# Kernel optimization log

Measured on AMD Instinct MI355X. Metric: run time of the kernel, lower is better.

Reference implementation:

```python
import jax, jax.numpy as jnp
import numpy as np

TAU = 0.5  # matches init_kwargs tau
EPS = 1e-8  # torch CosineSimilarity eps


def setup_inputs() -> dict:
    key = jax.random.key(0)
    k1, k2 = jax.random.split(key)
    B, D = 4096, 256
    return {
        "z_orig": jax.random.normal(k1, (B, D), dtype=jnp.float32),
        "z_augment": jax.random.normal(k2, (B, D), dtype=jnp.float32),
    }


def reference(z_orig, z_augment):
    B = z_orig.shape[0]
    N = 2 * B
    # collect_z = cat([z_augment, z_orig])  -> [2B, D]
    z = jnp.concatenate([z_augment, z_orig], axis=0)
    # cosine similarity matrix via L2 normalize + matmul
    zn = z / jnp.maximum(jnp.linalg.norm(z, axis=-1, keepdims=True), EPS)
    S = zn @ zn.T  # [2B, 2B]
    # positives: diag offsets +B and -B
    pos = jnp.concatenate([jnp.diagonal(S, B), jnp.diagonal(S, -B)])[:, None]  # [2B, 1]
    # negatives: everything except main diag and the +/-B diagonals.
    # Static indices (shape-dependent only), computed in numpy at trace time.
    mask = ~((np.eye(N, k=B) + np.eye(N, k=-B) + np.eye(N)).astype(bool))
    flat_idx = jnp.asarray(np.nonzero(mask.reshape(-1))[0])  # [2B*(2B-2)]
    neg = S.reshape(-1)[flat_idx].reshape(N, N - 2)  # row-major order matches torch boolean mask
    logits = jnp.concatenate([pos, neg], axis=1) / TAU  # [2B, 2B-1]
    # CrossEntropy with label 0 for every row, reduction='sum', then / 2B
    loss = -jax.nn.log_softmax(logits, axis=-1)[:, 0]
    return jnp.sum(loss) / N
```

## Files before the change

### kernel.cpp

```cpp
#include <hip/hip_runtime.h>
#include <hip/hip_bf16.h>

typedef __attribute__((ext_vector_type(4))) float f32x4;
typedef __attribute__((ext_vector_type(4))) int   i32x4;
typedef __attribute__((ext_vector_type(8))) int   i32x8;

#define N_ROWS 8192
#define B_HALF 4096
#define NUT   2080
#define EXP2C4 0.01127105500694503f
#define SCL1   0x7F7F7F7Fu

#define WS_ZN       0
#define WS_ROWACC   2097152
#define WS_POS      2129920
#define WS_DIAG     2162688
#define WS_ACC      2195456
#define WS_CNT      2195460

__device__ __forceinline__ float fexp2(float x) {
#if __has_builtin(__builtin_amdgcn_exp2f)
    return __builtin_amdgcn_exp2f(x);
#else
    return exp2f(x);
#endif
}

__device__ __forceinline__ unsigned int q4(float x) {
    float a = fabsf(x);
    unsigned int s = (__float_as_uint(x) >> 31) << 3;
    unsigned int c = a < 0.25f ? 0u : a < 0.75f ? 1u : a < 1.25f ? 2u
                   : a < 1.75f ? 3u : a < 2.5f  ? 4u : a < 3.5f  ? 5u
                   : a < 5.0f  ? 6u : 7u;
    return c | s;
}

__device__ __forceinline__ i32x8 widen(i32x4 v) {
    return (i32x8){v.x, v.y, v.z, v.w, 0, 0, 0, 0};
}

__device__ __forceinline__ float dpp_rowsum16(float x) {
    x += __int_as_float(__builtin_amdgcn_update_dpp(
             0, __float_as_int(x), 0x111, 0xF, 0xF, true));
    x += __int_as_float(__builtin_amdgcn_update_dpp(
             0, __float_as_int(x), 0x112, 0xF, 0xF, true));
    x += __int_as_float(__builtin_amdgcn_update_dpp(
             0, __float_as_int(x), 0x114, 0xF, 0xF, true));
    x += __int_as_float(__builtin_amdgcn_update_dpp(
             0, __float_as_int(x), 0x118, 0xF, 0xF, true));
    return x;
}

__global__ __launch_bounds__(256) void normalize_k(
    const float* __restrict__ z_orig, const float* __restrict__ z_aug,
    unsigned char* __restrict__ zn, float* __restrict__ rowAcc,
    float* __restrict__ accum, unsigned int* __restrict__ cnt)
{
    if (blockIdx.x == 0 && threadIdx.x == 0) { *accum = 0.0f; *cnt = 0u; }
    const int row  = blockIdx.x * 4 + (threadIdx.x >> 6);
    const int lane = threadIdx.x & 63;
    if (lane == 0) rowAcc[row] = 0.0f;
    const float* src = (row < B_HALF) ? (z_aug  + (size_t)row * 256)
                                      : (z_orig + (size_t)(row - B_HALF) * 256);
    float4 v = ((const float4*)src)[lane];
    float ss = v.x*v.x + v.y*v.y + v.z*v.z + v.w*v.w;
    #pragma unroll
    for (int m = 1; m < 64; m <<= 1) ss += __shfl_xor(ss, m);
    float inv = 16.0f / fmaxf(sqrtf(ss), 1e-8f);
    unsigned int pk = q4(v.x * inv) | (q4(v.y * inv) << 4)
                    | (q4(v.z * inv) << 8) | (q4(v.w * inv) << 12);
    const int addr = ((row >> 4) << 11) | ((lane >> 5) << 10) | ((row & 15) << 6)
                   | (((lane >> 3) & 3) << 4) | ((lane & 7) << 1);
    *(unsigned short*)(zn + addr) = (unsigned short)pk;
}

__global__ __launch_bounds__(256, 3) void tile_k(
    const unsigned char* __restrict__ zn,
    float* __restrict__ rowAcc,
    float* __restrict__ posv,
    float* __restrict__ diagE)
{
    const int bid = blockIdx.x;
    int rb = (int)((129.0f - sqrtf(16641.0f - 8.0f * (float)bid)) * 0.5f);
    rb = rb < 0 ? 0 : (rb > 63 ? 63 : rb);
    while ((rb + 1) * (129 - (rb + 1)) / 2 <= bid) ++rb;
    while (rb * (129 - rb) / 2 > bid) --rb;
    const int cb = rb + (bid - rb * (129 - rb) / 2);

    const int t      = threadIdx.x;
    const int lane   = t & 63;
    const int w      = t >> 6;
    const int wy     = w >> 1;
    const int wx     = w & 1;
    const int lane15 = lane & 15;
    const int quad   = lane >> 4;
    const int rowBase = rb * 128;
    const int colBase = cb * 128;

    const int laneOff = lane15 * 64 + quad * 16;
    const unsigned char* gA = zn + (size_t)(rb * 8 + wy * 4) * 2048 + laneOff;
    const unsigned char* gB = zn + (size_t)(cb * 8 + wx * 4) * 2048 + laneOff;

    f32x4 acc[4][4];
    #pragma unroll
    for (int i = 0; i < 4; ++i)
        #pragma unroll
        for (int j = 0; j < 4; ++j)
            acc[i][j] = (f32x4){0.f, 0.f, 0.f, 0.f};

    #pragma unroll
    for (int ks = 0; ks < 2; ++ks) {
        i32x4 a[4], b[4];
        #pragma unroll
        for (int mi = 0; mi < 4; ++mi)
            a[mi] = *(const i32x4*)(gA + mi * 2048 + ks * 1024);
        #pragma unroll
        for (int ni = 0; ni < 4; ++ni)
            b[ni] = *(const i32x4*)(gB + ni * 2048 + ks * 1024);
        #pragma unroll
        for (int mi = 0; mi < 4; ++mi)
            #pragma unroll
            for (int ni = 0; ni < 4; ++ni)
                acc[mi][ni] = __builtin_amdgcn_mfma_scale_f32_16x16x128_f8f6f4(
                    widen(a[mi]), widen(b[ni]), acc[mi][ni],
                    4, 4,
                    0, SCL1, 0, SCL1);
    }

    const bool diagLane = (wy == wx) && ((lane15 >> 2) == quad);
    const int  rsel = lane15 & 3;
    if (cb == rb && diagLane) {
        #pragma unroll
        for (int mi = 0; mi < 4; ++mi) {
            int grow = rowBase + wy * 64 + mi * 16 + lane15;
            diagE[grow] = fexp2(acc[mi][mi][rsel] * EXP2C4);
        }
    }
    if (cb == rb + 32 && diagLane) {
        #pragma unroll
        for (int mi = 0; mi < 4; ++mi) {
            int grow = rowBase + wy * 64 + mi * 16 + lane15;
            float v = acc[mi][mi][rsel];
            posv[grow] = v;
            posv[grow + B_HALF] = v;
        }
    }

    #pragma unroll
    for (int mi = 0; mi < 4; ++mi)
        #pragma unroll
        for (int ni = 0; ni < 4; ++ni)
            #pragma unroll
            for (int r = 0; r < 4; ++r)
                acc[mi][ni][r] = fexp2(acc[mi][ni][r] * EXP2C4);

    #pragma unroll
    for (int mi = 0; mi < 4; ++mi)
        #pragma unroll
        for (int r = 0; r < 4; ++r) {
            float s = acc[mi][0][r] + acc[mi][1][r] + acc[mi][2][r] + acc[mi][3][r];
            s = dpp_rowsum16(s);
            if (lane15 == 15)
                atomicAdd(&rowAcc[rowBase + wy * 64 + mi * 16 + quad * 4 + r], s);
        }

    if (cb != rb) {
        #pragma unroll
        for (int ni = 0; ni < 4; ++ni) {
            float s = 0.0f;
            #pragma unroll
            for (int mi = 0; mi < 4; ++mi)
                s += acc[mi][ni][0] + acc[mi][ni][1] + acc[mi][ni][2] + acc[mi][ni][3];
            s += __shfl_xor(s, 16);
            s += __shfl_xor(s, 32);
            if (quad == 0)
                atomicAdd(&rowAcc[colBase + wx * 64 + ni * 16 + lane15], s);
        }
    }
}

__global__ __launch_bounds__(256) void loss_k(
    const float* __restrict__ rowAcc, const float* __restrict__ posv,
    const float* __restrict__ diagE, float* __restrict__ accum,
    unsigned int* __restrict__ cnt, float* __restrict__ out)
{
    const int i = blockIdx.x * 256 + threadIdx.x;
    float s = rowAcc[i] - diagE[i];
    float loss = __logf(s) - posv[i] * 0.0078125f;

    #pragma unroll
    for (int m = 1; m < 64; m <<= 1) loss += __shfl_xor(loss, m);
    __shared__ float red[4];
    if ((threadIdx.x & 63) == 0) red[threadIdx.x >> 6] = loss;
    __syncthreads();
    if (threadIdx.x == 0) {
        float bs = red[0] + red[1] + red[2] + red[3];
        atomicAdd(accum, bs);
        __threadfence();
        unsigned int old = atomicAdd(cnt, 1u);
        if (old == 31u) {
            __threadfence();
            float total = atomicAdd(accum, 0.0f);
            out[0] = total * (1.0f / (float)N_ROWS);
        }
    }
}

extern "C" void kernel_launch(void* const* d_in, const int* in_sizes, int n_in,
                              void* d_out, int out_size, void* d_ws, size_t ws_size,
                              hipStream_t stream) {
    const float* z_orig = (const float*)d_in[0];
    const float* z_aug  = (const float*)d_in[1];
    char* ws = (char*)d_ws;
    unsigned char* zn   = (unsigned char*)(ws + WS_ZN);
    float* rowAcc       = (float*)(ws + WS_ROWACC);
    float* posv         = (float*)(ws + WS_POS);
    float* diagE        = (float*)(ws + WS_DIAG);
    float* accum        = (float*)(ws + WS_ACC);
    unsigned int* cnt   = (unsigned int*)(ws + WS_CNT);

    normalize_k<<<N_ROWS / 4, 256, 0, stream>>>(z_orig, z_aug, zn, rowAcc, accum, cnt);
    tile_k<<<NUT, 256, 0, stream>>>(zn, rowAcc, posv, diagE);
    loss_k<<<N_ROWS / 256, 256, 0, stream>>>(rowAcc, posv, diagE, accum, cnt,
                                             (float*)d_out);
}
```

Before: 92.94 us.

## Process two column tiles per block, reusing A fragments and prefetching next B

```diff
diff --git a/kernel.cpp b/kernel.cpp
--- a/kernel.cpp
+++ b/kernel.cpp
@@ -7,7 +7,6 @@
 
 #define N_ROWS 8192
 #define B_HALF 4096
-#define NUT   2080
 #define EXP2C4 0.01127105500694503f
 #define SCL1   0x7F7F7F7Fu
 
@@ -74,18 +73,75 @@
     *(unsigned short*)(zn + addr) = (unsigned short)pk;
 }
 
-__global__ __launch_bounds__(256, 3) void tile_k(
+__device__ __forceinline__ void do_epilogue(
+    f32x4 (&acc)[4][4], const int cb, const int rb, const int rowBase,
+    const int wy, const int wx, const int lane15, const int quad,
+    const bool diagLane, const int rsel,
+    float* __restrict__ rowAcc, float* __restrict__ posv,
+    float* __restrict__ diagE)
+{
+    const int colBase = cb * 128;
+    if (cb == rb && diagLane) {
+        #pragma unroll
+        for (int mi = 0; mi < 4; ++mi) {
+            int grow = rowBase + wy * 64 + mi * 16 + lane15;
+            diagE[grow] = fexp2(acc[mi][mi][rsel] * EXP2C4);
+        }
+    }
+    if (cb == rb + 32 && diagLane) {
+        #pragma unroll
+        for (int mi = 0; mi < 4; ++mi) {
+            int grow = rowBase + wy * 64 + mi * 16 + lane15;
+            float v = acc[mi][mi][rsel];
+            posv[grow] = v;
+            posv[grow + B_HALF] = v;
+        }
+    }
+
+    #pragma unroll
+    for (int mi = 0; mi < 4; ++mi)
+        #pragma unroll
+        for (int ni = 0; ni < 4; ++ni)
+            #pragma unroll
+            for (int r = 0; r < 4; ++r)
+                acc[mi][ni][r] = fexp2(acc[mi][ni][r] * EXP2C4);
+
+    #pragma unroll
+    for (int mi = 0; mi < 4; ++mi)
+        #pragma unroll
+        for (int r = 0; r < 4; ++r) {
+            float s = acc[mi][0][r] + acc[mi][1][r] + acc[mi][2][r] + acc[mi][3][r];
+            s = dpp_rowsum16(s);
+            if (lane15 == 15)
+                atomicAdd(&rowAcc[rowBase + wy * 64 + mi * 16 + quad * 4 + r], s);
+        }
+
+    if (cb != rb) {
+        #pragma unroll
+        for (int ni = 0; ni < 4; ++ni) {
+            float s = 0.0f;
+            #pragma unroll
+            for (int mi = 0; mi < 4; ++mi)
+                s += acc[mi][ni][0] + acc[mi][ni][1] + acc[mi][ni][2] + acc[mi][ni][3];
+            s += __shfl_xor(s, 16);
+            s += __shfl_xor(s, 32);
+            if (quad == 0)
+                atomicAdd(&rowAcc[colBase + wx * 64 + ni * 16 + lane15], s);
+        }
+    }
+}
+
+__global__ __launch_bounds__(256, 2) void tile_k(
     const unsigned char* __restrict__ zn,
     float* __restrict__ rowAcc,
     float* __restrict__ posv,
     float* __restrict__ diagE)
 {
-    const int bid = blockIdx.x;
-    int rb = (int)((129.0f - sqrtf(16641.0f - 8.0f * (float)bid)) * 0.5f);
-    rb = rb < 0 ? 0 : (rb > 63 ? 63 : rb);
-    while ((rb + 1) * (129 - (rb + 1)) / 2 <= bid) ++rb;
-    while (rb * (129 - rb) / 2 > bid) --rb;
-    const int cb = rb + (bid - rb * (129 - rb) / 2);
+    const int rb  = blockIdx.y;
+    const int cb0 = rb + 2 * (int)blockIdx.x;
+    if (cb0 > 63) return;
+    const int cb1 = cb0 + 1;
+    const bool have1 = (cb1 <= 63);
 
     const int t      = threadIdx.x;
     const int lane   = t & 63;
@@ -95,11 +151,22 @@
     const int lane15 = lane & 15;
     const int quad   = lane >> 4;
     const int rowBase = rb * 128;
-    const int colBase = cb * 128;
+    const bool diagLane = (wy == wx) && ((lane15 >> 2) == quad);
+    const int  rsel = lane15 & 3;
 
     const int laneOff = lane15 * 64 + quad * 16;
-    const unsigned char* gA = zn + (size_t)(rb * 8 + wy * 4) * 2048 + laneOff;
-    const unsigned char* gB = zn + (size_t)(cb * 8 + wx * 4) * 2048 + laneOff;
+    const unsigned char* gA  = zn + (size_t)(rb  * 8 + wy * 4) * 2048 + laneOff;
+    const unsigned char* gB0 = zn + (size_t)(cb0 * 8 + wx * 4) * 2048 + laneOff;
+    const unsigned char* gB1 = zn + (size_t)(cb1 * 8 + wx * 4) * 2048 + laneOff;
+
+    i32x4 a[8], b0[8];
+    #pragma unroll
+    for (int mi = 0; mi < 4; ++mi)
+        #pragma unroll
+        for (int ks = 0; ks < 2; ++ks) {
+            a[mi * 2 + ks]  = *(const i32x4*)(gA  + mi * 2048 + ks * 1024);
+            b0[mi * 2 + ks] = *(const i32x4*)(gB0 + mi * 2048 + ks * 1024);
+        }
 
     f32x4 acc[4][4];
     #pragma unroll
@@ -109,73 +176,46 @@
             acc[i][j] = (f32x4){0.f, 0.f, 0.f, 0.f};
 
     #pragma unroll
-    for (int ks = 0; ks < 2; ++ks) {
-        i32x4 a[4], b[4];
-        #pragma unroll
-        for (int mi = 0; mi < 4; ++mi)
-            a[mi] = *(const i32x4*)(gA + mi * 2048 + ks * 1024);
-        #pragma unroll
-        for (int ni = 0; ni < 4; ++ni)
-            b[ni] = *(const i32x4*)(gB + ni * 2048 + ks * 1024);
+    for (int ks = 0; ks < 2; ++ks)
         #pragma unroll
         for (int mi = 0; mi < 4; ++mi)
             #pragma unroll
             for (int ni = 0; ni < 4; ++ni)
                 acc[mi][ni] = __builtin_amdgcn_mfma_scale_f32_16x16x128_f8f6f4(
-                    widen(a[mi]), widen(b[ni]), acc[mi][ni],
-                    4, 4,
-                    0, SCL1, 0, SCL1);
-    }
-
-    const bool diagLane = (wy == wx) && ((lane15 >> 2) == quad);
-    const int  rsel = lane15 & 3;
-    if (cb == rb && diagLane) {
-        #pragma unroll
-        for (int mi = 0; mi < 4; ++mi) {
-            int grow = rowBase + wy * 64 + mi * 16 + lane15;
-            diagE[grow] = fexp2(acc[mi][mi][rsel] * EXP2C4);
-        }
-    }
-    if (cb == rb + 32 && diagLane) {
-        #pragma unroll
-        for (int mi = 0; mi < 4; ++mi) {
-            int grow = rowBase + wy * 64 + mi * 16 + lane15;
-            float v = acc[mi][mi][rsel];
-            posv[grow] = v;
-            posv[grow + B_HALF] = v;
-        }
-    }
-
-    #pragma unroll
-    for (int mi = 0; mi < 4; ++mi)
+                    widen(a[mi * 2 + ks]), widen(b0[ni * 2 + ks]), acc[mi][ni],
+                    4, 4, 0, SCL1, 0, SCL1);
+
+    i32x4 b1[8];
+    if (have1) {
         #pragma unroll
         for (int ni = 0; ni < 4; ++ni)
             #pragma unroll
-            for (int r = 0; r < 4; ++r)
-                acc[mi][ni][r] = fexp2(acc[mi][ni][r] * EXP2C4);
-
-    #pragma unroll
-    for (int mi = 0; mi < 4; ++mi)
-        #pragma unroll
-        for (int r = 0; r < 4; ++r) {
-            float s = acc[mi][0][r] + acc[mi][1][r] + acc[mi][2][r] + acc[mi][3][r];
-            s = dpp_rowsum16(s);
-            if (lane15 == 15)
-                atomicAdd(&rowAcc[rowBase + wy * 64 + mi * 16 + quad * 4 + r], s);
-        }
-
-    if (cb != rb) {
-        #pragma unroll
-        for (int ni = 0; ni < 4; ++ni) {
-            float s = 0.0f;
+            for (int ks = 0; ks < 2; ++ks)
+                b1[ni * 2 + ks] = *(const i32x4*)(gB1 + ni * 2048 + ks * 1024);
+    }
+
+    do_epilogue(acc, cb0, rb, rowBase, wy, wx, lane15, quad, diagLane, rsel,
+                rowAcc, posv, diagE);
+
+    if (have1) {
+        #pragma unroll
+        for (int i = 0; i < 4; ++i)
+            #pragma unroll
+            for (int j = 0; j < 4; ++j)
+                acc[i][j] = (f32x4){0.f, 0.f, 0.f, 0.f};
+
+        #pragma unroll
+        for (int ks = 0; ks < 2; ++ks)
             #pragma unroll
             for (int mi = 0; mi < 4; ++mi)
-                s += acc[mi][ni][0] + acc[mi][ni][1] + acc[mi][ni][2] + acc[mi][ni][3];
-            s += __shfl_xor(s, 16);
-            s += __shfl_xor(s, 32);
-            if (quad == 0)
-                atomicAdd(&rowAcc[colBase + wx * 64 + ni * 16 + lane15], s);
-        }
+                #pragma unroll
+                for (int ni = 0; ni < 4; ++ni)
+                    acc[mi][ni] = __builtin_amdgcn_mfma_scale_f32_16x16x128_f8f6f4(
+                        widen(a[mi * 2 + ks]), widen(b1[ni * 2 + ks]), acc[mi][ni],
+                        4, 4, 0, SCL1, 0, SCL1);
+
+        do_epilogue(acc, cb1, rb, rowBase, wy, wx, lane15, quad, diagLane, rsel,
+                    rowAcc, posv, diagE);
     }
 }
 
@@ -220,7 +260,7 @@
     unsigned int* cnt   = (unsigned int*)(ws + WS_CNT);
 
     normalize_k<<<N_ROWS / 4, 256, 0, stream>>>(z_orig, z_aug, zn, rowAcc, accum, cnt);
-    tile_k<<<NUT, 256, 0, stream>>>(zn, rowAcc, posv, diagE);
+    tile_k<<<dim3(32, 64), 256, 0, stream>>>(zn, rowAcc, posv, diagE);
     loss_k<<<N_ROWS / 256, 256, 0, stream>>>(rowAcc, posv, diagE, accum, cnt,
                                              (float*)d_out);
 }
```

Measured after the change: 116.2 us. 25.0% more time.
